# Kernel optimization log

Hardware: AMD Instinct MI355X
Metric: run time of the kernel (lower is better)

Reference implementation:

```python
import jax, jax.numpy as jnp
import numpy as np

B, NV, NQ = 8, 1024, 1024
VS = QS = OUT = 512
H = 8
DH = OUT // H


def setup_inputs() -> dict:
    key = jax.random.key(0)
    ks = jax.random.split(key, 8)
    s_in = 1.0 / np.sqrt(VS)
    s_cat = 1.0 / np.sqrt(OUT + VS)
    return {
        "v": jax.random.normal(ks[0], (B, NV, VS), jnp.float32),
        "q": jax.random.normal(ks[1], (B, NQ, QS), jnp.float32),
        "v_lin_w": jax.random.normal(ks[2], (VS, 3 * OUT), jnp.float32) * s_in,
        "v_lin_b": jnp.zeros((3 * OUT,), jnp.float32),
        "q_lin_w": jax.random.normal(ks[3], (QS, 3 * OUT), jnp.float32) * s_in,
        "q_lin_b": jnp.zeros((3 * OUT,), jnp.float32),
        "v_out_w": jax.random.normal(ks[4], (OUT + VS, OUT), jnp.float32) * s_cat,
        "v_out_b": jnp.zeros((OUT,), jnp.float32),
        "q_out_w": jax.random.normal(ks[5], (OUT + QS, OUT), jnp.float32) * s_cat,
        "q_out_b": jnp.zeros((OUT,), jnp.float32),
    }


def _heads(x, n):
    # [B, N, OUT] -> [B, N, H, DH]
    return x.reshape(x.shape[0], n, H, DH)


def reference(v, q, v_lin_w, v_lin_b, q_lin_w, q_lin_b,
              v_out_w, v_out_b, q_out_w, q_out_b):
    scale = jnp.asarray(DH, v.dtype) ** 0.5
    v_tran = jax.nn.relu(v @ v_lin_w + v_lin_b)  # [B,NV,3*OUT]
    q_tran = jax.nn.relu(q @ q_lin_w + q_lin_b)  # [B,NQ,3*OUT]
    v_key, v_query, v_val = jnp.split(v_tran, 3, axis=2)
    q_key, q_query, q_val = jnp.split(q_tran, 3, axis=2)
    vk, vq, vv = _heads(v_key, NV), _heads(v_query, NV), _heads(v_val, NV)
    qk, qq, qv = _heads(q_key, NQ), _heads(q_query, NQ), _heads(q_val, NQ)
    # v attends to q: scores [B,H,NV,NQ]
    q2v = jnp.einsum('bvhd,bqhd->bhvq', vq, qk) / scale
    a_q2v = jax.nn.softmax(q2v, axis=-1)
    v_update = jnp.einsum('bhvq,bqhd->bvhd', a_q2v, qv).reshape(B, NV, OUT)
    # q attends to v: scores [B,H,NQ,NV]
    v2q = jnp.einsum('bqhd,bvhd->bhqv', qq, vk) / scale
    a_v2q = jax.nn.softmax(v2q, axis=-1)
    q_update = jnp.einsum('bhqv,bvhd->bqhd', a_v2q, vv).reshape(B, NQ, OUT)
    cat_v = jnp.concatenate([v, v_update], axis=2)
    cat_q = jnp.concatenate([q, q_update], axis=2)
    updated_v = jax.nn.relu(cat_v @ v_out_w + v_out_b)
    updated_q = jax.nn.relu(cat_q @ q_out_w + q_out_b)
    return updated_v, updated_q
```

## Files before the change

kernel.cpp:

```cpp
#include <hip/hip_runtime.h>
#include <hip/hip_bf16.h>

#define B_    8
#define NV_   1024
#define NQ_   1024
#define OUT_  512
#define H_    8
#define DH_   64

typedef __attribute__((ext_vector_type(8))) short   bf16x8_t;
typedef __attribute__((ext_vector_type(4))) float   f32x4_t;

__device__ __forceinline__ ushort f2b(float f) {
  union { float f; unsigned u; } x{f};
  unsigned r = x.u + 0x7FFFu + ((x.u >> 16) & 1u);
  return (ushort)(r >> 16);
}

__global__ __launch_bounds__(256)
void transpose_cast_bf16(const float* __restrict__ W, ushort* __restrict__ WT,
                         int K, int N) {
  int gid = blockIdx.x * 256 + threadIdx.x;
  int total = (N * K) >> 3;
  if (gid >= total) return;
  int n = gid % N;
  int k0 = (gid / N) * 8;
  bf16x8_t pk;
#pragma unroll
  for (int i = 0; i < 8; ++i) pk[i] = (short)f2b(W[(size_t)(k0 + i) * N + n]);
  *(bf16x8_t*)(WT + (size_t)n * K + k0) = pk;
}

__global__ __launch_bounds__(256)
void transpose_val_bf16(const ushort* __restrict__ T, ushort* __restrict__ Vt,
                        int N) {
  __shared__ ushort tile[64][70];
  const int tid = threadIdx.x;
  const int nt = blockIdx.x, h = blockIdx.y, b = blockIdx.z;
  const ushort* src = T + ((size_t)(b * N + nt * 64)) * 1536 + 1024 + h * 64;
#pragma unroll
  for (int it = 0; it < 2; ++it) {
    int c = it * 256 + tid;
    int r = c >> 3;
    int cc = (c & 7) * 8;
    union { bf16x8_t v; uint u[4]; } x;
    x.v = *(const bf16x8_t*)(src + (size_t)r * 1536 + cc);
    uint* dst = (uint*)&tile[r][cc];
    dst[0] = x.u[0]; dst[1] = x.u[1]; dst[2] = x.u[2]; dst[3] = x.u[3];
  }
  __syncthreads();
  ushort* dstb = Vt + ((size_t)(b * H_ + h) * DH_) * N + nt * 64;
#pragma unroll
  for (int it = 0; it < 2; ++it) {
    int t = it * 256 + tid;
    int d = t >> 3;
    int ns = (t & 7) * 8;
    bf16x8_t o;
#pragma unroll
    for (int i = 0; i < 8; ++i) o[i] = (short)tile[ns + i][d];
    *(bf16x8_t*)(dstb + (size_t)d * N + ns) = o;
  }
}

template<bool OUT_BF16>
__global__ __launch_bounds__(256)
void gemm_mfma_bias_relu(const float* __restrict__ A1, int lda1,
                         const float* __restrict__ A2, int lda2, int ksplit,
                         const ushort* __restrict__ WT,
                         const float* __restrict__ bias,
                         void* __restrict__ Cv, int ldc,
                         int M, int N, int K) {
  constexpr int BM = 128, BN = 128, BK = 32;
  constexpr int LK = BK + 8;
  __shared__ ushort As[BM][LK];
  __shared__ ushort Bs[BN][LK];

  const int tid = threadIdx.x;
  const int l   = tid & 63;
  const int wid = tid >> 6;
  const int wr  = wid >> 1;
  const int wc  = wid & 1;
  const int fr  = l & 15;
  const int k8  = (l >> 4) * 8;
  const int bm  = blockIdx.y * BM;
  const int bn  = blockIdx.x * BN;

  f32x4_t acc[4][4];
#pragma unroll
  for (int mi = 0; mi < 4; ++mi)
#pragma unroll
    for (int ni = 0; ni < 4; ++ni) acc[mi][ni] = (f32x4_t){0.f, 0.f, 0.f, 0.f};

  for (int k0 = 0; k0 < K; k0 += BK) {
#pragma unroll
    for (int it = 0; it < 2; ++it) {
      int c   = it * 256 + tid;
      int row = c >> 2;
      int kk  = (c & 3) * 8;
      int gk  = k0 + kk;
      const float* src = (gk < ksplit)
          ? A1 + (size_t)(bm + row) * lda1 + gk
          : A2 + (size_t)(bm + row) * lda2 + (gk - ksplit);
      float4 f0 = *(const float4*)src;
      float4 f1 = *(const float4*)(src + 4);
      bf16x8_t pk;
      pk[0] = (short)f2b(f0.x); pk[1] = (short)f2b(f0.y);
      pk[2] = (short)f2b(f0.z); pk[3] = (short)f2b(f0.w);
      pk[4] = (short)f2b(f1.x); pk[5] = (short)f2b(f1.y);
      pk[6] = (short)f2b(f1.z); pk[7] = (short)f2b(f1.w);
      *(bf16x8_t*)&As[row][kk] = pk;
    }
#pragma unroll
    for (int it = 0; it < 2; ++it) {
      int c   = it * 256 + tid;
      int n   = c >> 2;
      int kk  = (c & 3) * 8;
      *(bf16x8_t*)&Bs[n][kk] =
          *(const bf16x8_t*)(WT + (size_t)(bn + n) * K + k0 + kk);
    }
    __syncthreads();

    bf16x8_t af[4], bfr[4];
#pragma unroll
    for (int mi = 0; mi < 4; ++mi)
      af[mi] = *(bf16x8_t*)&As[wr * 64 + mi * 16 + fr][k8];
#pragma unroll
    for (int ni = 0; ni < 4; ++ni)
      bfr[ni] = *(bf16x8_t*)&Bs[wc * 64 + ni * 16 + fr][k8];
#pragma unroll
    for (int mi = 0; mi < 4; ++mi)
#pragma unroll
      for (int ni = 0; ni < 4; ++ni)
        acc[mi][ni] = __builtin_amdgcn_mfma_f32_16x16x32_bf16(
            af[mi], bfr[ni], acc[mi][ni], 0, 0, 0);
    __syncthreads();
  }

  const int rq = (l >> 4) * 4;
#pragma unroll
  for (int ni = 0; ni < 4; ++ni) {
    const int col = bn + wc * 64 + ni * 16 + fr;
    const float bv = bias[col];
#pragma unroll
    for (int mi = 0; mi < 4; ++mi) {
#pragma unroll
      for (int r = 0; r < 4; ++r) {
        const int row = bm + wr * 64 + mi * 16 + rq + r;
        const float val = fmaxf(acc[mi][ni][r] + bv, 0.f);
        if (OUT_BF16)
          ((ushort*)Cv)[(size_t)row * ldc + col] = f2b(val);
        else
          ((float*)Cv)[(size_t)row * ldc + col] = val;
      }
    }
  }
}

__global__ __launch_bounds__(256)
void flash_attn_mfma(const ushort* __restrict__ Qg, int ldq,
                     const ushort* __restrict__ Kg, int ldk,
                     const ushort* __restrict__ Vtg,
                     float* __restrict__ Ug, int ldu,
                     int Nq, int Nk) {
  constexpr int LS = 72;
  __shared__ ushort QPs[64][LS];
  __shared__ ushort Ks[64][LS];
  __shared__ ushort Vts[64][LS];
  const int tid = threadIdx.x;
  const int l   = tid & 63;
  const int w   = tid >> 6;
  const int fr  = l & 15;
  const int k8  = (l >> 4) * 8;
  const int rq  = (l >> 4) * 4;
  const int bid = blockIdx.x + 16 * (blockIdx.y + 8 * blockIdx.z);
  const int L   = (bid & 7) * 128 + (bid >> 3);
  const int qt  = L & 15;
  const int h   = (L >> 4) & 7;
  const int b   = L >> 7;
  const int i0  = qt * 64;
  const ushort* Qb  = Qg + ((size_t)b * Nq + i0) * ldq + h * DH_;
  const ushort* Kb  = Kg + ((size_t)b * Nk) * ldk + h * DH_;
  const ushort* Vtb = Vtg + ((size_t)(b * H_ + h) * DH_) * Nk;

#pragma unroll
  for (int it = 0; it < 2; ++it) {
    int c = it * 256 + tid;
    int row = c >> 3;
    int col = (c & 7) * 8;
    *(bf16x8_t*)&QPs[row][col] = *(const bf16x8_t*)(Qb + (size_t)row * ldq + col);
  }
  __syncthreads();
  const bf16x8_t aq0 = *(bf16x8_t*)&QPs[16 * w + fr][k8];
  const bf16x8_t aq1 = *(bf16x8_t*)&QPs[16 * w + fr][32 + k8];

  float m[4], lsum[4];
  f32x4_t accO[4];
#pragma unroll
  for (int r = 0; r < 4; ++r) { m[r] = -1e30f; lsum[r] = 0.f; }
#pragma unroll
  for (int di = 0; di < 4; ++di) accO[di] = (f32x4_t){0.f, 0.f, 0.f, 0.f};

  for (int j0 = 0; j0 < Nk; j0 += 64) {
    __syncthreads();
#pragma unroll
    for (int it = 0; it < 2; ++it) {
      int c = it * 256 + tid;
      int row = c >> 3;
      int col = (c & 7) * 8;
      *(bf16x8_t*)&Ks[row][col] =
          *(const bf16x8_t*)(Kb + (size_t)(j0 + row) * ldk + col);
      *(bf16x8_t*)&Vts[row][col] =
          *(const bf16x8_t*)(Vtb + (size_t)row * Nk + j0 + col);
    }
    __syncthreads();

    f32x4_t accS[4];
#pragma unroll
    for (int ni = 0; ni < 4; ++ni) accS[ni] = (f32x4_t){0.f, 0.f, 0.f, 0.f};
#pragma unroll
    for (int ni = 0; ni < 4; ++ni) {
      bf16x8_t bk = *(bf16x8_t*)&Ks[ni * 16 + fr][k8];
      accS[ni] = __builtin_amdgcn_mfma_f32_16x16x32_bf16(aq0, bk, accS[ni], 0, 0, 0);
    }
#pragma unroll
    for (int ni = 0; ni < 4; ++ni) {
      bf16x8_t bk = *(bf16x8_t*)&Ks[ni * 16 + fr][32 + k8];
      accS[ni] = __builtin_amdgcn_mfma_f32_16x16x32_bf16(aq1, bk, accS[ni], 0, 0, 0);
    }

#pragma unroll
    for (int r = 0; r < 4; ++r) {
      float s0 = accS[0][r] * 0.125f;
      float s1 = accS[1][r] * 0.125f;
      float s2 = accS[2][r] * 0.125f;
      float s3 = accS[3][r] * 0.125f;
      float t = fmaxf(fmaxf(s0, s1), fmaxf(s2, s3));
      t = fmaxf(t, __shfl_xor(t, 1));
      t = fmaxf(t, __shfl_xor(t, 2));
      t = fmaxf(t, __shfl_xor(t, 4));
      t = fmaxf(t, __shfl_xor(t, 8));
      float mn = fmaxf(m[r], t);
      float fac = __expf(m[r] - mn);
      m[r] = mn;
      float p0 = __expf(s0 - mn);
      float p1 = __expf(s1 - mn);
      float p2 = __expf(s2 - mn);
      float p3 = __expf(s3 - mn);
      float ts = (p0 + p1) + (p2 + p3);
      ts += __shfl_xor(ts, 1);
      ts += __shfl_xor(ts, 2);
      ts += __shfl_xor(ts, 4);
      ts += __shfl_xor(ts, 8);
      lsum[r] = lsum[r] * fac + ts;
#pragma unroll
      for (int di = 0; di < 4; ++di) accO[di][r] *= fac;
      const int prow = 16 * w + rq + r;
      QPs[prow][fr +  0] = f2b(p0);
      QPs[prow][fr + 16] = f2b(p1);
      QPs[prow][fr + 32] = f2b(p2);
      QPs[prow][fr + 48] = f2b(p3);
    }
    asm volatile("s_waitcnt lgkmcnt(0)" ::: "memory");
    __builtin_amdgcn_sched_barrier(0);

#pragma unroll
    for (int kk = 0; kk < 64; kk += 32) {
      bf16x8_t pa = *(bf16x8_t*)&QPs[16 * w + fr][kk + k8];
#pragma unroll
      for (int di = 0; di < 4; ++di) {
        bf16x8_t vb = *(bf16x8_t*)&Vts[di * 16 + fr][kk + k8];
        accO[di] = __builtin_amdgcn_mfma_f32_16x16x32_bf16(pa, vb, accO[di], 0, 0, 0);
      }
    }
  }

#pragma unroll
  for (int r = 0; r < 4; ++r) {
    float inv = 1.f / lsum[r];
    float* urow = Ug + ((size_t)b * Nq + i0 + 16 * w + rq + r) * ldu + h * DH_;
#pragma unroll
    for (int di = 0; di < 4; ++di)
      urow[di * 16 + fr] = accO[di][r] * inv;
  }
}

extern "C" void kernel_launch(void* const* d_in, const int* in_sizes, int n_in,
                              void* d_out, int out_size, void* d_ws, size_t ws_size,
                              hipStream_t stream) {
  const float* v        = (const float*)d_in[0];
  const float* q        = (const float*)d_in[1];
  const float* v_lin_w  = (const float*)d_in[2];
  const float* v_lin_b  = (const float*)d_in[3];
  const float* q_lin_w  = (const float*)d_in[4];
  const float* q_lin_b  = (const float*)d_in[5];
  const float* v_out_w  = (const float*)d_in[6];
  const float* v_out_b  = (const float*)d_in[7];
  const float* q_out_w  = (const float*)d_in[8];
  const float* q_out_b  = (const float*)d_in[9];
  float* out = (float*)d_out;

  const int M = B_ * NV_;

  const size_t ws_needed =
      (size_t)2 * M * 1536 * 2 + (size_t)2 * M * 512 * 4 +
      ((size_t)2 * 512 * 1536 + (size_t)2 * 1024 * 512) * 2 +
      (size_t)2 * B_ * H_ * DH_ * 1024 * 2;
  if (ws_size < ws_needed) return;

  ushort* v_tranb = (ushort*)d_ws;
  ushort* q_tranb = v_tranb + (size_t)M * 1536;
  float*  v_upd   = (float*)(q_tranb + (size_t)M * 1536);
  float*  q_upd   = v_upd + (size_t)M * 512;
  ushort* vlwT    = (ushort*)(q_upd + (size_t)M * 512);
  ushort* qlwT    = vlwT + (size_t)512 * 1536;
  ushort* vowT    = qlwT + (size_t)512 * 1536;
  ushort* qowT    = vowT + (size_t)1024 * 512;
  ushort* vvt     = qowT + (size_t)1024 * 512;
  ushort* qvt     = vvt  + (size_t)B_ * H_ * DH_ * 1024;

  dim3 blk(256);

  transpose_cast_bf16<<<dim3((512 * 1536 / 8 + 255) / 256), blk, 0, stream>>>(
      v_lin_w, vlwT, 512, 1536);
  transpose_cast_bf16<<<dim3((512 * 1536 / 8 + 255) / 256), blk, 0, stream>>>(
      q_lin_w, qlwT, 512, 1536);
  transpose_cast_bf16<<<dim3((1024 * 512 / 8 + 255) / 256), blk, 0, stream>>>(
      v_out_w, vowT, 1024, 512);
  transpose_cast_bf16<<<dim3((1024 * 512 / 8 + 255) / 256), blk, 0, stream>>>(
      q_out_w, qowT, 1024, 512);

  {
    dim3 grid(1536 / 128, M / 128);
    (gemm_mfma_bias_relu<true>)<<<grid, blk, 0, stream>>>(
        v, 512, v, 512, 512, vlwT, v_lin_b, v_tranb, 1536, M, 1536, 512);
    (gemm_mfma_bias_relu<true>)<<<grid, blk, 0, stream>>>(
        q, 512, q, 512, 512, qlwT, q_lin_b, q_tranb, 1536, M, 1536, 512);
  }

  {
    dim3 grid(NV_ / 64, H_, B_);
    transpose_val_bf16<<<grid, blk, 0, stream>>>(v_tranb, vvt, NV_);
    transpose_val_bf16<<<grid, blk, 0, stream>>>(q_tranb, qvt, NQ_);
  }

  {
    dim3 grid(NV_ / 64, H_, B_);
    flash_attn_mfma<<<grid, blk, 0, stream>>>(
        v_tranb + 512, 1536, q_tranb, 1536, qvt, v_upd, 512, NV_, NQ_);
    flash_attn_mfma<<<grid, blk, 0, stream>>>(
        q_tranb + 512, 1536, v_tranb, 1536, vvt, q_upd, 512, NQ_, NV_);
  }

  {
    dim3 grid(512 / 128, M / 128);
    (gemm_mfma_bias_relu<false>)<<<grid, blk, 0, stream>>>(
        v, 512, v_upd, 512, 512, vowT, v_out_b, out, 512, M, 512, 1024);
    (gemm_mfma_bias_relu<false>)<<<grid, blk, 0, stream>>>(
        q, 512, q_upd, 512, 512, qowT, q_out_b,
        out + (size_t)M * 512, 512, M, 512, 1024);
  }
}
```

Measured before the change: 370.5 us.

## Pre-cast inputs to bf16 and load GEMM tiles directly into LDS

Adds a cast kernel that converts v and q to bf16 once. The GEMMs now read bf16 A operands through global_load_lds, removing the per-tile float-to-bf16 conversion and the register round trip. The attention outputs are also stored in bf16, which halves that traffic for the output GEMM, and workgroups are remapped in an XCD-aware order. The GEMM LDS tiles lose their padding, which can cause bank conflicts. Each loop iteration now has a single barrier placed before the loads, and the attention update is now rounded to bf16.

```diff
diff --git a/kernel.cpp b/kernel.cpp
--- a/kernel.cpp
+++ b/kernel.cpp
@@ -15,6 +15,26 @@
   union { float f; unsigned u; } x{f};
   unsigned r = x.u + 0x7FFFu + ((x.u >> 16) & 1u);
   return (ushort)(r >> 16);
+}
+
+__device__ __forceinline__ void gload_lds16(const ushort* g, ushort* l) {
+  __builtin_amdgcn_global_load_lds(
+      (const __attribute__((address_space(1))) void*)g,
+      (__attribute__((address_space(3))) void*)l, 16, 0, 0);
+}
+
+__global__ __launch_bounds__(256)
+void cast_f32_bf16(const float* __restrict__ x, ushort* __restrict__ y, int n8) {
+  int i = blockIdx.x * 256 + threadIdx.x;
+  if (i >= n8) return;
+  float4 a = ((const float4*)x)[2 * i];
+  float4 b = ((const float4*)x)[2 * i + 1];
+  bf16x8_t pk;
+  pk[0] = (short)f2b(a.x); pk[1] = (short)f2b(a.y);
+  pk[2] = (short)f2b(a.z); pk[3] = (short)f2b(a.w);
+  pk[4] = (short)f2b(b.x); pk[5] = (short)f2b(b.y);
+  pk[6] = (short)f2b(b.z); pk[7] = (short)f2b(b.w);
+  ((bf16x8_t*)y)[i] = pk;
 }
 
 __global__ __launch_bounds__(256)
@@ -64,16 +84,14 @@
 
 template<bool OUT_BF16>
 __global__ __launch_bounds__(256)
-void gemm_mfma_bias_relu(const float* __restrict__ A1, int lda1,
-                         const float* __restrict__ A2, int lda2, int ksplit,
-                         const ushort* __restrict__ WT,
-                         const float* __restrict__ bias,
-                         void* __restrict__ Cv, int ldc,
-                         int M, int N, int K) {
-  constexpr int BM = 128, BN = 128, BK = 32;
-  constexpr int LK = BK + 8;
-  __shared__ ushort As[BM][LK];
-  __shared__ ushort Bs[BN][LK];
+void gemm_mfma_bf16(const ushort* __restrict__ A1, int lda1,
+                    const ushort* __restrict__ A2, int lda2, int ksplit,
+                    const ushort* __restrict__ WT,
+                    const float* __restrict__ bias,
+                    void* __restrict__ Cv, int ldc,
+                    int M, int N, int K, int nbx) {
+  __shared__ ushort As[128][32];
+  __shared__ ushort Bs[128][32];
 
   const int tid = threadIdx.x;
   const int l   = tid & 63;
@@ -82,8 +100,14 @@
   const int wc  = wid & 1;
   const int fr  = l & 15;
   const int k8  = (l >> 4) * 8;
-  const int bm  = blockIdx.y * BM;
-  const int bn  = blockIdx.x * BN;
+  const int nwg   = nbx * gridDim.y;
+  const int bid   = blockIdx.y * nbx + blockIdx.x;
+  const int chunk = nwg >> 3;
+  const int L     = (bid & 7) * chunk + (bid >> 3);
+  const int bm    = (L / nbx) * 128;
+  const int bn    = (L % nbx) * 128;
+  const int srow  = l >> 2;
+  const int scol  = (l & 3) * 8;
 
   f32x4_t acc[4][4];
 #pragma unroll
@@ -91,32 +115,18 @@
 #pragma unroll
     for (int ni = 0; ni < 4; ++ni) acc[mi][ni] = (f32x4_t){0.f, 0.f, 0.f, 0.f};
 
-  for (int k0 = 0; k0 < K; k0 += BK) {
+  for (int k0 = 0; k0 < K; k0 += 32) {
+    __syncthreads();
 #pragma unroll
     for (int it = 0; it < 2; ++it) {
-      int c   = it * 256 + tid;
-      int row = c >> 2;
-      int kk  = (c & 3) * 8;
-      int gk  = k0 + kk;
-      const float* src = (gk < ksplit)
+      const int row = it * 64 + wid * 16 + srow;
+      const int gk  = k0 + scol;
+      const ushort* asrc = (gk < ksplit)
           ? A1 + (size_t)(bm + row) * lda1 + gk
           : A2 + (size_t)(bm + row) * lda2 + (gk - ksplit);
-      float4 f0 = *(const float4*)src;
-      float4 f1 = *(const float4*)(src + 4);
-      bf16x8_t pk;
-      pk[0] = (short)f2b(f0.x); pk[1] = (short)f2b(f0.y);
-      pk[2] = (short)f2b(f0.z); pk[3] = (short)f2b(f0.w);
-      pk[4] = (short)f2b(f1.x); pk[5] = (short)f2b(f1.y);
-      pk[6] = (short)f2b(f1.z); pk[7] = (short)f2b(f1.w);
-      *(bf16x8_t*)&As[row][kk] = pk;
-    }
-#pragma unroll
-    for (int it = 0; it < 2; ++it) {
-      int c   = it * 256 + tid;
-      int n   = c >> 2;
-      int kk  = (c & 3) * 8;
-      *(bf16x8_t*)&Bs[n][kk] =
-          *(const bf16x8_t*)(WT + (size_t)(bn + n) * K + k0 + kk);
+      gload_lds16(asrc, &As[0][0] + (size_t)(it * 64 + wid * 16) * 32);
+      const ushort* bsrc = WT + (size_t)(bn + row) * K + gk;
+      gload_lds16(bsrc, &Bs[0][0] + (size_t)(it * 64 + wid * 16) * 32);
     }
     __syncthreads();
 
@@ -133,7 +143,6 @@
       for (int ni = 0; ni < 4; ++ni)
         acc[mi][ni] = __builtin_amdgcn_mfma_f32_16x16x32_bf16(
             af[mi], bfr[ni], acc[mi][ni], 0, 0, 0);
-    __syncthreads();
   }
 
   const int rq = (l >> 4) * 4;
@@ -160,7 +169,7 @@
 void flash_attn_mfma(const ushort* __restrict__ Qg, int ldq,
                      const ushort* __restrict__ Kg, int ldk,
                      const ushort* __restrict__ Vtg,
-                     float* __restrict__ Ug, int ldu,
+                     ushort* __restrict__ Ug, int ldu,
                      int Nq, int Nk) {
   constexpr int LS = 72;
   __shared__ ushort QPs[64][LS];
@@ -277,10 +286,10 @@
 #pragma unroll
   for (int r = 0; r < 4; ++r) {
     float inv = 1.f / lsum[r];
-    float* urow = Ug + ((size_t)b * Nq + i0 + 16 * w + rq + r) * ldu + h * DH_;
+    ushort* urow = Ug + ((size_t)b * Nq + i0 + 16 * w + rq + r) * ldu + h * DH_;
 #pragma unroll
     for (int di = 0; di < 4; ++di)
-      urow[di * 16 + fr] = accO[di][r] * inv;
+      urow[di * 16 + fr] = f2b(accO[di][r] * inv);
   }
 }
 
@@ -302,16 +311,20 @@
   const int M = B_ * NV_;
 
   const size_t ws_needed =
-      (size_t)2 * M * 1536 * 2 + (size_t)2 * M * 512 * 4 +
+      (size_t)2 * M * 512 * 2 +
+      (size_t)2 * M * 1536 * 2 +
+      (size_t)2 * M * 512 * 2 +
       ((size_t)2 * 512 * 1536 + (size_t)2 * 1024 * 512) * 2 +
       (size_t)2 * B_ * H_ * DH_ * 1024 * 2;
   if (ws_size < ws_needed) return;
 
-  ushort* v_tranb = (ushort*)d_ws;
+  ushort* vb      = (ushort*)d_ws;
+  ushort* qb      = vb + (size_t)M * 512;
+  ushort* v_tranb = qb + (size_t)M * 512;
   ushort* q_tranb = v_tranb + (size_t)M * 1536;
-  float*  v_upd   = (float*)(q_tranb + (size_t)M * 1536);
-  float*  q_upd   = v_upd + (size_t)M * 512;
-  ushort* vlwT    = (ushort*)(q_upd + (size_t)M * 512);
+  ushort* v_updb  = q_tranb + (size_t)M * 1536;
+  ushort* q_updb  = v_updb + (size_t)M * 512;
+  ushort* vlwT    = q_updb + (size_t)M * 512;
   ushort* qlwT    = vlwT + (size_t)512 * 1536;
   ushort* vowT    = qlwT + (size_t)512 * 1536;
   ushort* qowT    = vowT + (size_t)1024 * 512;
@@ -320,21 +333,23 @@
 
   dim3 blk(256);
 
-  transpose_cast_bf16<<<dim3((512 * 1536 / 8 + 255) / 256), blk, 0, stream>>>(
+  cast_f32_bf16<<<dim3(M * 512 / 8 / 256), blk, 0, stream>>>(v, vb, M * 512 / 8);
+  cast_f32_bf16<<<dim3(M * 512 / 8 / 256), blk, 0, stream>>>(q, qb, M * 512 / 8);
+  transpose_cast_bf16<<<dim3(512 * 1536 / 8 / 256), blk, 0, stream>>>(
       v_lin_w, vlwT, 512, 1536);
-  transpose_cast_bf16<<<dim3((512 * 1536 / 8 + 255) / 256), blk, 0, stream>>>(
+  transpose_cast_bf16<<<dim3(512 * 1536 / 8 / 256), blk, 0, stream>>>(
       q_lin_w, qlwT, 512, 1536);
-  transpose_cast_bf16<<<dim3((1024 * 512 / 8 + 255) / 256), blk, 0, stream>>>(
+  transpose_cast_bf16<<<dim3(1024 * 512 / 8 / 256), blk, 0, stream>>>(
       v_out_w, vowT, 1024, 512);
-  transpose_cast_bf16<<<dim3((1024 * 512 / 8 + 255) / 256), blk, 0, stream>>>(
+  transpose_cast_bf16<<<dim3(1024 * 512 / 8 / 256), blk, 0, stream>>>(
       q_out_w, qowT, 1024, 512);
 
   {
     dim3 grid(1536 / 128, M / 128);
-    (gemm_mfma_bias_relu<true>)<<<grid, blk, 0, stream>>>(
-        v, 512, v, 512, 512, vlwT, v_lin_b, v_tranb, 1536, M, 1536, 512);
-    (gemm_mfma_bias_relu<true>)<<<grid, blk, 0, stream>>>(
-        q, 512, q, 512, 512, qlwT, q_lin_b, q_tranb, 1536, M, 1536, 512);
+    (gemm_mfma_bf16<true>)<<<grid, blk, 0, stream>>>(
+        vb, 512, vb, 512, 512, vlwT, v_lin_b, v_tranb, 1536, M, 1536, 512, 12);
+    (gemm_mfma_bf16<true>)<<<grid, blk, 0, stream>>>(
+        qb, 512, qb, 512, 512, qlwT, q_lin_b, q_tranb, 1536, M, 1536, 512, 12);
   }
 
   {
@@ -346,17 +361,17 @@
   {
     dim3 grid(NV_ / 64, H_, B_);
     flash_attn_mfma<<<grid, blk, 0, stream>>>(
-        v_tranb + 512, 1536, q_tranb, 1536, qvt, v_upd, 512, NV_, NQ_);
+        v_tranb + 512, 1536, q_tranb, 1536, qvt, v_updb, 512, NV_, NQ_);
     flash_attn_mfma<<<grid, blk, 0, stream>>>(
-        q_tranb + 512, 1536, v_tranb, 1536, vvt, q_upd, 512, NQ_, NV_);
+        q_tranb + 512, 1536, v_tranb, 1536, vvt, q_updb, 512, NQ_, NV_);
   }
 
   {
     dim3 grid(512 / 128, M / 128);
-    (gemm_mfma_bias_relu<false>)<<<grid, blk, 0, stream>>>(
-        v, 512, v_upd, 512, 512, vowT, v_out_b, out, 512, M, 512, 1024);
-    (gemm_mfma_bias_relu<false>)<<<grid, blk, 0, stream>>>(
-        q, 512, q_upd, 512, 512, qowT, q_out_b,
-        out + (size_t)M * 512, 512, M, 512, 1024);
-  }
-}
+    (gemm_mfma_bf16<false>)<<<grid, blk, 0, stream>>>(
+        vb, 512, v_updb, 512, 512, vowT, v_out_b, out, 512, M, 512, 1024, 4);
+    (gemm_mfma_bf16<false>)<<<grid, blk, 0, stream>>>(
+        qb, 512, q_updb, 512, 512, qowT, q_out_b,
+        out + (size_t)M * 512, 512, M, 512, 1024, 4);
+  }
+}
```

Result: faster. 343.7 us (-7.2%).
